# Optimization experiments

Measured on AMD Instinct MI355X. Metric: run time of the kernel, lower is better.

The kernel has to match this reference:

```python
import jax, jax.numpy as jnp
import numpy as np

N_ENT = 50000
N_REL = 500
N_EDGE = 800000
H_DIM = 96
BN_EPS = 1e-5


def setup_inputs() -> dict:
    key = jax.random.key(0)
    k1, k2, k3, k4, k5 = jax.random.split(key, 5)
    return {
        "ent_emb": jax.random.normal(k1, (N_ENT, H_DIM), dtype=jnp.float32),
        "rel_emb": jax.random.normal(k2, (N_REL, H_DIM), dtype=jnp.float32),
        "neigh_w": jax.random.normal(k3, (H_DIM, H_DIM), dtype=jnp.float32) * (1.0 / np.sqrt(H_DIM)),
        "bn_gamma": jnp.ones((H_DIM,), dtype=jnp.float32),
        "bn_beta": jnp.zeros((H_DIM,), dtype=jnp.float32),
        "rel_id": jax.random.randint(k4, (N_EDGE,), 0, N_REL, dtype=jnp.int64),
        "dst": jax.random.randint(k5, (N_EDGE,), 0, N_ENT, dtype=jnp.int64),
    }


def reference(ent_emb, rel_emb, neigh_w, bn_gamma, bn_beta, rel_id, dst):
    n_nodes = ent_emb.shape[0]
    # per-edge gather: edge feature = relation embedding  [E, D]
    e = rel_emb[rel_id]
    # e_dot_v: dot of edge feature with destination node embedding  [E]
    score = jnp.sum(e * ent_emb[dst], axis=-1)
    # edge softmax over incoming edges of each destination node
    seg_max = jax.ops.segment_max(score, dst, num_segments=n_nodes)  # [N]
    w = jnp.exp(score - seg_max[dst])                                # [E]
    seg_sum = jax.ops.segment_sum(w, dst, num_segments=n_nodes)      # [N]
    alpha = w / seg_sum[dst]                                         # [E]
    # weighted scatter-sum aggregation into destination nodes  [N, D]
    neigh = jax.ops.segment_sum(e * alpha[:, None], dst, num_segments=n_nodes)
    # linear
    out = neigh @ neigh_w
    # BatchNorm1d (training mode: batch stats over nodes, biased var)
    mu = jnp.mean(out, axis=0)
    var = jnp.mean((out - mu) ** 2, axis=0)
    out = (out - mu) * jax.lax.rsqrt(var + BN_EPS) * bn_gamma + bn_beta
    return jnp.tanh(out)
```

## Files before the change

### kernel.cpp

```cpp
#include <hip/hip_runtime.h>
#include <math.h>

#define N_ENT   50000
#define N_REL   500
#define N_EDGE  800000
#define H       96
#define BN_EPS  1e-5f
#define DEG_CAP 64
#define NCOPY   32
#define NBLK_NODE 2048
#define NGRP    ((N_ENT + 3) / 4)
#define SM_SHIFT 24.0f

#define RELW_BLOCKS ((N_REL * H + 255) / 256)
#define ZERO_N      (N_ENT + NCOPY * 2 * H)
#define ZERO_BLOCKS ((ZERO_N + 255) / 256)

__global__ __launch_bounds__(256) void k_init(
        const float* __restrict__ rel, const float* __restrict__ W,
        float* __restrict__ relW, unsigned* __restrict__ zbase) {
    if (blockIdx.x < RELW_BLOCKS) {
        __shared__ float Ws[H * H];
        for (int i = threadIdx.x; i < H * H; i += 256) Ws[i] = W[i];
        __syncthreads();
        int t = blockIdx.x * 256 + threadIdx.x;
        if (t >= N_REL * H) return;
        int r = t / H;
        int c = t - r * H;
        const float4* rr = (const float4*)(rel + (size_t)r * H);
        float acc = 0.0f;
#pragma unroll
        for (int i = 0; i < H / 4; ++i) {
            float4 a = rr[i];
            acc += a.x * Ws[(4 * i + 0) * H + c];
            acc += a.y * Ws[(4 * i + 1) * H + c];
            acc += a.z * Ws[(4 * i + 2) * H + c];
            acc += a.w * Ws[(4 * i + 3) * H + c];
        }
        relW[t] = acc;
    } else {
        int i = (blockIdx.x - RELW_BLOCKS) * 256 + threadIdx.x;
        if (i < ZERO_N) zbase[i] = 0u;
    }
}

__global__ __launch_bounds__(256) void k_bucket(
        const int* __restrict__ dst, const int* __restrict__ rel_id,
        int* __restrict__ cursor, unsigned short* __restrict__ pay) {
    int e = blockIdx.x * 256 + threadIdx.x;
    if (e >= N_EDGE) return;
    int d = dst[e];
    int r = rel_id[e];
    int p = atomicAdd(cursor + d, 1);
    if (p < DEG_CAP) pay[d * DEG_CAP + p] = (unsigned short)r;
}

__global__ __launch_bounds__(256) void k_node(
        const float* __restrict__ ent, const float* __restrict__ rel,
        const unsigned short* __restrict__ pay, const int* __restrict__ cursor,
        const float* __restrict__ relW, float* __restrict__ out,
        float* __restrict__ bn_part) {
    __shared__ float sh_e[4][DEG_CAP];
    __shared__ float sh_red[4][2 * H];
    int wv   = threadIdx.x >> 6;
    int lane = threadIdx.x & 63;
    int g  = lane & 7;
    int es = lane >> 3;

    float4 s0 = make_float4(0.f,0.f,0.f,0.f), s1 = s0, s2 = s0;
    float4 q0 = s0, q1 = s0, q2 = s0;

    int grp = blockIdx.x;
    int cnt_c, rid_c;
    {
        int n0 = grp * 4 + wv;
        cnt_c = cursor[n0];
        rid_c = (int)pay[(size_t)n0 * DEG_CAP + lane];
    }
    while (grp < NGRP) {
        int grp_nx = grp + (int)gridDim.x;
        int cnt_nx = 0, rid_nx = 0;
        if (grp_nx < NGRP) {
            int nn = grp_nx * 4 + wv;
            cnt_nx = cursor[nn];
            rid_nx = (int)pay[(size_t)nn * DEG_CAP + lane];
        }
        int n   = grp * 4 + wv;
        int cnt = min(cnt_c, DEG_CAP);
        int myrid = (lane < cnt) ? rid_c : 0;

        {
            int qd = lane & 3;
            int jj = lane >> 2;
            const float4* er = (const float4*)(ent + (size_t)n * H) + qd * 6;
            float4 e0 = er[0], e1 = er[1], e2 = er[2], e3 = er[3], e4 = er[4], e5 = er[5];
            int npass = (cnt + 15) >> 4;
            for (int p = 0; p < npass; ++p) {
                int j = (p << 4) + jj;
                int rid = __shfl(myrid, j);
                bool valid = (j < cnt);
                float part = 0.0f;
                const float4* rr = (const float4*)(rel + (size_t)rid * H) + qd * 6;
                float4 b;
                b = rr[0]; part += e0.x*b.x + e0.y*b.y + e0.z*b.z + e0.w*b.w;
                b = rr[1]; part += e1.x*b.x + e1.y*b.y + e1.z*b.z + e1.w*b.w;
                b = rr[2]; part += e2.x*b.x + e2.y*b.y + e2.z*b.z + e2.w*b.w;
                b = rr[3]; part += e3.x*b.x + e3.y*b.y + e3.z*b.z + e3.w*b.w;
                b = rr[4]; part += e4.x*b.x + e4.y*b.y + e4.z*b.z + e4.w*b.w;
                b = rr[5]; part += e5.x*b.x + e5.y*b.y + e5.z*b.z + e5.w*b.w;
                part += __shfl_xor(part, 1);
                part += __shfl_xor(part, 2);
                if (valid && qd == 0) sh_e[wv][j] = __expf(part - SM_SHIFT);
            }
        }

        int rj0 = __shfl(myrid, es);
        int rj1 = __shfl(myrid, es + 8);
        const float4* p0 = (const float4*)(relW + (size_t)rj0 * H + g * 12);
        const float4* p1 = (const float4*)(relW + (size_t)rj1 * H + g * 12);
        float4 f00 = p0[0], f01 = p0[1], f02 = p0[2];
        float4 f10 = p1[0], f11 = p1[1], f12 = p1[2];

        float alpha;
        {
            float ej = (lane < cnt) ? sh_e[wv][lane] : 0.0f;
            float s = ej;
#pragma unroll
            for (int off = 1; off < 64; off <<= 1)
                s += __shfl_xor(s, off);
            float inv = (cnt > 0) ? 1.0f / s : 0.0f;
            alpha = ej * inv;
        }

        float w0 = __shfl(alpha, es);
        float w1 = __shfl(alpha, es + 8);
        float4 a0, a1, a2;
        a0.x = w0*f00.x + w1*f10.x; a0.y = w0*f00.y + w1*f10.y;
        a0.z = w0*f00.z + w1*f10.z; a0.w = w0*f00.w + w1*f10.w;
        a1.x = w0*f01.x + w1*f11.x; a1.y = w0*f01.y + w1*f11.y;
        a1.z = w0*f01.z + w1*f11.z; a1.w = w0*f01.w + w1*f11.w;
        a2.x = w0*f02.x + w1*f12.x; a2.y = w0*f02.y + w1*f12.y;
        a2.z = w0*f02.z + w1*f12.z; a2.w = w0*f02.w + w1*f12.w;

        int rem = cnt - 16;
        int npass2 = (rem > 0) ? ((rem + 7) >> 3) : 0;
        for (int m2 = 0; m2 < npass2; ++m2) {
            int k = es + 16 + (m2 << 3);
            int rid = __shfl(myrid, k);
            float w = __shfl(alpha, k);
            const float4* p = (const float4*)(relW + (size_t)rid * H + g * 12);
            float4 f0 = p[0], f1 = p[1], f2 = p[2];
            a0.x += w * f0.x; a0.y += w * f0.y; a0.z += w * f0.z; a0.w += w * f0.w;
            a1.x += w * f1.x; a1.y += w * f1.y; a1.z += w * f1.z; a1.w += w * f1.w;
            a2.x += w * f2.x; a2.y += w * f2.y; a2.z += w * f2.z; a2.w += w * f2.w;
        }
#pragma unroll
        for (int off = 8; off < 64; off <<= 1) {
            a0.x += __shfl_xor(a0.x, off); a0.y += __shfl_xor(a0.y, off);
            a0.z += __shfl_xor(a0.z, off); a0.w += __shfl_xor(a0.w, off);
            a1.x += __shfl_xor(a1.x, off); a1.y += __shfl_xor(a1.y, off);
            a1.z += __shfl_xor(a1.z, off); a1.w += __shfl_xor(a1.w, off);
            a2.x += __shfl_xor(a2.x, off); a2.y += __shfl_xor(a2.y, off);
            a2.z += __shfl_xor(a2.z, off); a2.w += __shfl_xor(a2.w, off);
        }
        if (es == 0) {
            float4* op = (float4*)(out + (size_t)n * H + g * 12);
            op[0] = a0; op[1] = a1; op[2] = a2;
            s0.x += a0.x; s0.y += a0.y; s0.z += a0.z; s0.w += a0.w;
            s1.x += a1.x; s1.y += a1.y; s1.z += a1.z; s1.w += a1.w;
            s2.x += a2.x; s2.y += a2.y; s2.z += a2.z; s2.w += a2.w;
            q0.x += a0.x*a0.x; q0.y += a0.y*a0.y; q0.z += a0.z*a0.z; q0.w += a0.w*a0.w;
            q1.x += a1.x*a1.x; q1.y += a1.y*a1.y; q1.z += a1.z*a1.z; q1.w += a1.w*a1.w;
            q2.x += a2.x*a2.x; q2.y += a2.y*a2.y; q2.z += a2.z*a2.z; q2.w += a2.w*a2.w;
        }
        grp = grp_nx; cnt_c = cnt_nx; rid_c = rid_nx;
    }

    if (es == 0) {
        float4* ps = (float4*)(&sh_red[wv][g * 12]);
        ps[0] = s0; ps[1] = s1; ps[2] = s2;
        float4* pq = (float4*)(&sh_red[wv][H + g * 12]);
        pq[0] = q0; pq[1] = q1; pq[2] = q2;
    }
    __syncthreads();
    int t = threadIdx.x;
    if (t < 2 * H) {
        float tot = sh_red[0][t] + sh_red[1][t] + sh_red[2][t] + sh_red[3][t];
        atomicAdd(bn_part + (blockIdx.x & (NCOPY - 1)) * (2 * H) + t, tot);
    }
}

__device__ __forceinline__ float fast_tanh(float x) {
    return 1.0f - 2.0f / (__expf(2.0f * x) + 1.0f);
}

__global__ __launch_bounds__(256) void k_bnapply(
        float* __restrict__ out, const float* __restrict__ bn_part,
        const float* __restrict__ gamma, const float* __restrict__ beta) {
    __shared__ float sA[H], sB[H];
    int t = threadIdx.x;
    if (t < H) {
        float s = 0.0f, qq = 0.0f;
#pragma unroll
        for (int c = 0; c < NCOPY; ++c) {
            s  += bn_part[c * (2 * H) + t];
            qq += bn_part[c * (2 * H) + H + t];
        }
        const float inv_n = 1.0f / (float)N_ENT;
        float mu = s * inv_n;
        float r  = rsqrtf(qq * inv_n - mu * mu + BN_EPS);
        float gg = gamma[t];
        float a  = r * gg;
        sA[t] = a;
        sB[t] = beta[t] - mu * a;
    }
    __syncthreads();
    int idx = blockIdx.x * 256 + t;
    if (idx >= N_ENT * H / 4) return;
    int c4 = idx % (H / 4);
    float4 v = ((const float4*)out)[idx];
    float4 o;
    o.x = fast_tanh(v.x * sA[4 * c4 + 0] + sB[4 * c4 + 0]);
    o.y = fast_tanh(v.y * sA[4 * c4 + 1] + sB[4 * c4 + 1]);
    o.z = fast_tanh(v.z * sA[4 * c4 + 2] + sB[4 * c4 + 2]);
    o.w = fast_tanh(v.w * sA[4 * c4 + 3] + sB[4 * c4 + 3]);
    ((float4*)out)[idx] = o;
}

extern "C" void kernel_launch(void* const* d_in, const int* in_sizes, int n_in,
                              void* d_out, int out_size, void* d_ws, size_t ws_size,
                              hipStream_t stream) {
    const float* ent   = (const float*)d_in[0];
    const float* rel   = (const float*)d_in[1];
    const float* W     = (const float*)d_in[2];
    const float* gamma = (const float*)d_in[3];
    const float* beta  = (const float*)d_in[4];
    const int* rel_id  = (const int*)d_in[5];
    const int* dst     = (const int*)d_in[6];
    float* out = (float*)d_out;

    float* ws       = (float*)d_ws;
    int*   cursor   = (int*)ws;
    float* bn_part  = ws + N_ENT;
    float* relW     = bn_part + NCOPY * 2 * H;
    unsigned short* pay = (unsigned short*)(relW + N_REL * H);

    k_init<<<RELW_BLOCKS + ZERO_BLOCKS, 256, 0, stream>>>(
        rel, W, relW, (unsigned*)cursor);
    k_bucket<<<(N_EDGE + 255) / 256, 256, 0, stream>>>(dst, rel_id, cursor, pay);
    k_node<<<NBLK_NODE, 256, 0, stream>>>(ent, rel, pay, cursor, relW, out,
                                          bn_part);
    k_bnapply<<<(N_ENT * H / 4 + 255) / 256, 256, 0, stream>>>(
        out, bn_part, gamma, beta);
}
```

Before: 193.4 us.

## Aggregate relW rows per lane via shared (alpha, rid) pairs instead of shuffle reductions

```diff
diff --git a/kernel.cpp b/kernel.cpp
--- a/kernel.cpp
+++ b/kernel.cpp
@@ -60,15 +60,13 @@
         const unsigned short* __restrict__ pay, const int* __restrict__ cursor,
         const float* __restrict__ relW, float* __restrict__ out,
         float* __restrict__ bn_part) {
-    __shared__ float sh_e[4][DEG_CAP];
-    __shared__ float sh_red[4][2 * H];
+    __shared__ float4 sh_er[4][DEG_CAP / 2];
+    __shared__ float  sh_red[4][2 * H];
     int wv   = threadIdx.x >> 6;
     int lane = threadIdx.x & 63;
-    int g  = lane & 7;
-    int es = lane >> 3;
-
-    float4 s0 = make_float4(0.f,0.f,0.f,0.f), s1 = s0, s2 = s0;
-    float4 q0 = s0, q1 = s0, q2 = s0;
+
+    float2 bsum = make_float2(0.f, 0.f);
+    float2 bsq  = make_float2(0.f, 0.f);
 
     int grp = blockIdx.x;
     int cnt_c, rid_c;
@@ -88,13 +86,13 @@
         int n   = grp * 4 + wv;
         int cnt = min(cnt_c, DEG_CAP);
         int myrid = (lane < cnt) ? rid_c : 0;
+        int npass = (cnt + 15) >> 4;
 
         {
             int qd = lane & 3;
             int jj = lane >> 2;
             const float4* er = (const float4*)(ent + (size_t)n * H) + qd * 6;
             float4 e0 = er[0], e1 = er[1], e2 = er[2], e3 = er[3], e4 = er[4], e5 = er[5];
-            int npass = (cnt + 15) >> 4;
             for (int p = 0; p < npass; ++p) {
                 int j = (p << 4) + jj;
                 int rid = __shfl(myrid, j);
@@ -110,77 +108,54 @@
                 b = rr[5]; part += e5.x*b.x + e5.y*b.y + e5.z*b.z + e5.w*b.w;
                 part += __shfl_xor(part, 1);
                 part += __shfl_xor(part, 2);
-                if (valid && qd == 0) sh_e[wv][j] = __expf(part - SM_SHIFT);
+                if (valid && qd == 0) {
+                    float2* wr = (float2*)&sh_er[wv][0];
+                    wr[j] = make_float2(__expf(part - SM_SHIFT),
+                                        __int_as_float(rid));
+                }
             }
         }
 
-        int rj0 = __shfl(myrid, es);
-        int rj1 = __shfl(myrid, es + 8);
-        const float4* p0 = (const float4*)(relW + (size_t)rj0 * H + g * 12);
-        const float4* p1 = (const float4*)(relW + (size_t)rj1 * H + g * 12);
-        float4 f00 = p0[0], f01 = p0[1], f02 = p0[2];
-        float4 f10 = p1[0], f11 = p1[1], f12 = p1[2];
-
-        float alpha;
+        float inv;
         {
-            float ej = (lane < cnt) ? sh_e[wv][lane] : 0.0f;
+            const float2* rd = (const float2*)&sh_er[wv][0];
+            float ej = (lane < cnt) ? rd[lane].x : 0.0f;
             float s = ej;
 #pragma unroll
             for (int off = 1; off < 64; off <<= 1)
                 s += __shfl_xor(s, off);
-            float inv = (cnt > 0) ? 1.0f / s : 0.0f;
-            alpha = ej * inv;
-        }
-
-        float w0 = __shfl(alpha, es);
-        float w1 = __shfl(alpha, es + 8);
-        float4 a0, a1, a2;
-        a0.x = w0*f00.x + w1*f10.x; a0.y = w0*f00.y + w1*f10.y;
-        a0.z = w0*f00.z + w1*f10.z; a0.w = w0*f00.w + w1*f10.w;
-        a1.x = w0*f01.x + w1*f11.x; a1.y = w0*f01.y + w1*f11.y;
-        a1.z = w0*f01.z + w1*f11.z; a1.w = w0*f01.w + w1*f11.w;
-        a2.x = w0*f02.x + w1*f12.x; a2.y = w0*f02.y + w1*f12.y;
-        a2.z = w0*f02.z + w1*f12.z; a2.w = w0*f02.w + w1*f12.w;
-
-        int rem = cnt - 16;
-        int npass2 = (rem > 0) ? ((rem + 7) >> 3) : 0;
-        for (int m2 = 0; m2 < npass2; ++m2) {
-            int k = es + 16 + (m2 << 3);
-            int rid = __shfl(myrid, k);
-            float w = __shfl(alpha, k);
-            const float4* p = (const float4*)(relW + (size_t)rid * H + g * 12);
-            float4 f0 = p[0], f1 = p[1], f2 = p[2];
-            a0.x += w * f0.x; a0.y += w * f0.y; a0.z += w * f0.z; a0.w += w * f0.w;
-            a1.x += w * f1.x; a1.y += w * f1.y; a1.z += w * f1.z; a1.w += w * f1.w;
-            a2.x += w * f2.x; a2.y += w * f2.y; a2.z += w * f2.z; a2.w += w * f2.w;
-        }
-#pragma unroll
-        for (int off = 8; off < 64; off <<= 1) {
-            a0.x += __shfl_xor(a0.x, off); a0.y += __shfl_xor(a0.y, off);
-            a0.z += __shfl_xor(a0.z, off); a0.w += __shfl_xor(a0.w, off);
-            a1.x += __shfl_xor(a1.x, off); a1.y += __shfl_xor(a1.y, off);
-            a1.z += __shfl_xor(a1.z, off); a1.w += __shfl_xor(a1.w, off);
-            a2.x += __shfl_xor(a2.x, off); a2.y += __shfl_xor(a2.y, off);
-            a2.z += __shfl_xor(a2.z, off); a2.w += __shfl_xor(a2.w, off);
-        }
-        if (es == 0) {
-            float4* op = (float4*)(out + (size_t)n * H + g * 12);
-            op[0] = a0; op[1] = a1; op[2] = a2;
-            s0.x += a0.x; s0.y += a0.y; s0.z += a0.z; s0.w += a0.w;
-            s1.x += a1.x; s1.y += a1.y; s1.z += a1.z; s1.w += a1.w;
-            s2.x += a2.x; s2.y += a2.y; s2.z += a2.z; s2.w += a2.w;
-            q0.x += a0.x*a0.x; q0.y += a0.y*a0.y; q0.z += a0.z*a0.z; q0.w += a0.w*a0.w;
-            q1.x += a1.x*a1.x; q1.y += a1.y*a1.y; q1.z += a1.z*a1.z; q1.w += a1.w*a1.w;
-            q2.x += a2.x*a2.x; q2.y += a2.y*a2.y; q2.z += a2.z*a2.z; q2.w += a2.w*a2.w;
+            inv = (cnt > 0) ? 1.0f / s : 0.0f;
+        }
+
+        if (lane < 48) {
+            float2 acc = make_float2(0.f, 0.f);
+            const float2* relW2 = (const float2*)relW;
+            for (int p = 0; p < npass; ++p) {
+#pragma unroll
+                for (int i = 0; i < 8; ++i) {
+                    int k0 = (p << 4) + 2 * i;
+                    float4 pr = sh_er[wv][(p << 3) + i];
+                    bool v0 = (k0 < cnt), v1 = (k0 + 1 < cnt);
+                    float al0 = v0 ? pr.x * inv : 0.0f;
+                    float al1 = v1 ? pr.z * inv : 0.0f;
+                    int r0 = v0 ? __float_as_int(pr.y) : 0;
+                    int r1 = v1 ? __float_as_int(pr.w) : 0;
+                    float2 f0 = relW2[r0 * 48 + lane];
+                    float2 f1 = relW2[r1 * 48 + lane];
+                    acc.x += al0 * f0.x + al1 * f1.x;
+                    acc.y += al0 * f0.y + al1 * f1.y;
+                }
+            }
+            ((float2*)(out + (size_t)n * H))[lane] = acc;
+            bsum.x += acc.x; bsum.y += acc.y;
+            bsq.x  += acc.x * acc.x; bsq.y += acc.y * acc.y;
         }
         grp = grp_nx; cnt_c = cnt_nx; rid_c = rid_nx;
     }
 
-    if (es == 0) {
-        float4* ps = (float4*)(&sh_red[wv][g * 12]);
-        ps[0] = s0; ps[1] = s1; ps[2] = s2;
-        float4* pq = (float4*)(&sh_red[wv][H + g * 12]);
-        pq[0] = q0; pq[1] = q1; pq[2] = q2;
+    if (lane < 48) {
+        ((float2*)&sh_red[wv][0])[lane] = bsum;
+        ((float2*)&sh_red[wv][H])[lane] = bsq;
     }
     __syncthreads();
     int t = threadIdx.x;
```

Result: slower. 208.5 us (+7.8%).
